# Optimization experiments

Hardware: AMD Instinct MI355X
Metric: run time of the kernel (lower is better)

Reference implementation:

```python
import jax, jax.numpy as jnp
import numpy as np

N_NODES = 50000
N_EDGES = 640000
D = 128
BN_EPS = 1e-5


def setup_inputs() -> dict:
    key = jax.random.key(0)
    k1, k2, k3 = jax.random.split(key, 3)
    x = jax.random.normal(k1, (N_NODES, D), dtype=jnp.float32)
    # Glorot-ish weight for GCNConv linear
    W = jax.random.normal(k2, (D, D), dtype=jnp.float32) * (1.0 / np.sqrt(D))
    b = jnp.zeros((D,), dtype=jnp.float32)
    gamma = jnp.ones((D,), dtype=jnp.float32)
    beta = jnp.zeros((D,), dtype=jnp.float32)
    edge_index = jax.random.randint(k3, (2, N_EDGES), 0, N_NODES, dtype=jnp.int64)
    return {"x": x, "W": W, "b": b, "gamma": gamma, "beta": beta, "edge_index": edge_index}


def reference(x, W, b, gamma, beta, edge_index):
    N = x.shape[0]
    # --- GCNConv: x' = D^{-1/2} (A + I) D^{-1/2} (x W) + b ---
    xw = x @ W  # [N, D]
    loops = jnp.arange(N, dtype=edge_index.dtype)
    src = jnp.concatenate([edge_index[0], loops])  # [E+N]
    dst = jnp.concatenate([edge_index[1], loops])
    ones = jnp.ones(src.shape[0], dtype=x.dtype)
    deg = jax.ops.segment_sum(ones, dst, num_segments=N)  # in-degree incl. self-loop
    dinv = jnp.where(deg > 0, jax.lax.rsqrt(deg), 0.0)
    norm = dinv[src] * dinv[dst]  # [E+N]
    msg = xw[src] * norm[:, None]  # [E+N, D] gathered + scaled messages
    h = jax.ops.segment_sum(msg, dst, num_segments=N) + b  # scatter-add aggregation
    # --- BatchNorm1d (training-mode batch stats over nodes, biased var) ---
    mean = jnp.mean(h, axis=0)
    var = jnp.mean(jnp.square(h - mean), axis=0)
    h = (h - mean) * jax.lax.rsqrt(var + BN_EPS) * gamma + beta
    # --- activation (relu) ---
    h = jax.nn.relu(h)
    # --- residual (in_channels == out_channels) ---
    h = x + h
    # --- dropout: identity in eval mode for deterministic reference ---
    return h
```

## Files before the change

kernel.cpp:

```cpp
#include <hip/hip_runtime.h>

#define DCH 128
#define ROWS 16
#define BN_EPS 1e-5f

typedef unsigned short u16;
typedef __attribute__((ext_vector_type(8))) short short8;
typedef __attribute__((ext_vector_type(4))) float floatx4;
typedef __attribute__((ext_vector_type(2))) unsigned uint2v;

__device__ __forceinline__ float bf2f(u16 u) {
    return __uint_as_float(((unsigned)u) << 16);
}
__device__ __forceinline__ u16 f2bf(float f) {
    unsigned u = __float_as_uint(f);
    u += 0x7FFFu + ((u >> 16) & 1u);
    return (u16)(u >> 16);
}
__device__ __forceinline__ float ldf(const void* p, int i, int isbf) {
    return isbf ? bf2f(((const u16*)p)[i]) : ((const float*)p)[i];
}

__global__ void prep_kernel(const int* ei, int ewords, const u16* xw, int* ws_i,
                            const void* W, u16* Wb, float* zbase, int zn) {
    int t = threadIdx.x;
    __shared__ int s_nz, s_hits;
    if (t == 0) { s_nz = 0; s_hits = 0; }
    __syncthreads();
    if (blockIdx.x == 0) {
        int nz = 0;
        for (int i = t; i < 1024; i += 256) {
            int w = 2 * i + 1;
            if (w < ewords) nz |= ei[w];
        }
        if (nz) atomicOr(&s_nz, 1);
    }
    unsigned m = (xw[2 * t] >> 8) & 0x7F;
    if (m >= 0x3B && m <= 0x43) atomicAdd(&s_hits, 1);
    __syncthreads();
    int isbf = (s_hits >= 128) ? 1 : 0;
    if (blockIdx.x == 0 && t == 0) {
        ws_i[0] = (s_nz == 0) ? 1 : 0;
        ws_i[1] = isbf;
        ws_i[2] = 0;
    }
    int gstride = gridDim.x * 256;
    for (int idx = blockIdx.x * 256 + t; idx < DCH * DCH; idx += gstride) {
        int j = idx & 7, lane = (idx >> 3) & 63, kk = (idx >> 9) & 3, nt = idx >> 11;
        int k = kk * 32 + (lane >> 4) * 8 + j;
        int n = nt * 16 + (lane & 15);
        Wb[idx] = f2bf(ldf(W, k * DCH + n, isbf));
    }
    for (int i = blockIdx.x * 256 + t; i < zn; i += gstride) zbase[i] = 0.f;
}

__global__ void zero_kernel(float* p, int n) {
    int stride = gridDim.x * 256;
    for (int i = blockIdx.x * 256 + threadIdx.x; i < n; i += stride) p[i] = 0.f;
}

__global__ void paint_kernel(u16* out, int n, unsigned val) {
    int stride = gridDim.x * 256;
    for (int i = blockIdx.x * 256 + threadIdx.x; i < n; i += stride) out[i] = (u16)val;
}

__global__ void detect_kernel(const int* ei, int ewords, const u16* xw, int* ws_i) {
    __shared__ int s_nz, s_hits;
    int t = threadIdx.x;
    if (t == 0) { s_nz = 0; s_hits = 0; }
    __syncthreads();
    int nz = 0;
    for (int i = t; i < 1024; i += 256) {
        int w = 2 * i + 1;
        if (w < ewords) nz |= ei[w];
    }
    if (nz) atomicOr(&s_nz, 1);
    unsigned m = (xw[2 * t] >> 8) & 0x7F;
    if (m >= 0x3B && m <= 0x43) atomicAdd(&s_hits, 1);
    __syncthreads();
    if (t == 0) {
        ws_i[0] = (s_nz == 0) ? 1 : 0;
        ws_i[1] = (s_hits >= 128) ? 1 : 0;
        ws_i[2] = 0;
    }
}

__global__ void deg_kernel(const int* ei, int E, int* ws_i, int* deg, int N) {
    int is64 = ws_i[0];
    int i = blockIdx.x * 256 + threadIdx.x;
    if (i < E) {
        int s = is64 ? ei[2 * i] : ei[i];
        int d = is64 ? ei[2 * E + 2 * i] : ei[E + i];
        if (((unsigned)s >= (unsigned)N) || ((unsigned)d >= (unsigned)N))
            atomicOr(&ws_i[2], 2);
        d = min(max(d, 0), N - 1);
        atomicAdd(&deg[d], 1);
    }
}

__global__ void dinv_kernel(const int* deg, float* dinv, int N, int* ws_i) {
    int i = blockIdx.x * 256 + threadIdx.x;
    if (i < N) {
        float v = rsqrtf((float)(deg[i] + 1));
        if (!(v > 0.f && v <= 1.001f)) atomicOr(&ws_i[2], 4);
        dinv[i] = v;
    }
}

__global__ void scanA_kernel(const int* deg, int* part, int N) {
    int base = blockIdx.x * 1024 + threadIdx.x * 4;
    int s = 0;
    #pragma unroll
    for (int j = 0; j < 4; ++j) {
        int i = base + j;
        if (i < N) s += deg[i];
    }
    #pragma unroll
    for (int o = 1; o < 64; o <<= 1) s += __shfl_xor(s, o, 64);
    __shared__ int ws4[4];
    if ((threadIdx.x & 63) == 0) ws4[threadIdx.x >> 6] = s;
    __syncthreads();
    if (threadIdx.x == 0) part[blockIdx.x] = ws4[0] + ws4[1] + ws4[2] + ws4[3];
}

__global__ void scanB_kernel(int* part, int P) {
    __shared__ int wsum[4];
    int t = threadIdx.x, lane = t & 63, w = t >> 6;
    int v = (t < P) ? part[t] : 0;
    int sc = v;
    #pragma unroll
    for (int o = 1; o < 64; o <<= 1) {
        int u = __shfl_up(sc, o, 64);
        if (lane >= o) sc += u;
    }
    if (lane == 63) wsum[w] = sc;
    __syncthreads();
    if (t < 4) {
        int s = wsum[t];
        #pragma unroll
        for (int o = 1; o < 4; o <<= 1) {
            int u = __shfl_up(s, o, 4);
            if (t >= o) s += u;
        }
        wsum[t] = s;
    }
    __syncthreads();
    int excl = sc - v + (w ? wsum[w - 1] : 0);
    if (t < P) part[t] = excl;
}

__global__ void scanC_kernel(int* deg_cursor, const int* part, int* rowptr,
                             float* dinv, int N) {
    __shared__ int wsum[4];
    int t = threadIdx.x, lane = t & 63, w = t >> 6;
    int base = blockIdx.x * 1024 + t * 4;
    int v[4], ts = 0;
    #pragma unroll
    for (int j = 0; j < 4; ++j) {
        int i = base + j;
        v[j] = (i < N) ? deg_cursor[i] : 0;
        ts += v[j];
    }
    int sc = ts;
    #pragma unroll
    for (int o = 1; o < 64; o <<= 1) {
        int u = __shfl_up(sc, o, 64);
        if (lane >= o) sc += u;
    }
    if (lane == 63) wsum[w] = sc;
    __syncthreads();
    if (t < 4) {
        int s = wsum[t];
        #pragma unroll
        for (int o = 1; o < 4; o <<= 1) {
            int u = __shfl_up(s, o, 4);
            if (t >= o) s += u;
        }
        wsum[t] = s;
    }
    __syncthreads();
    int run = sc - ts + (w ? wsum[w - 1] : 0) + part[blockIdx.x];
    #pragma unroll
    for (int j = 0; j < 4; ++j) {
        int i = base + j;
        if (i < N) {
            deg_cursor[i] = run;
            run += v[j];
            rowptr[i + 1] = run;
            dinv[i] = rsqrtf((float)(v[j] + 1));
        }
    }
    if (blockIdx.x == 0 && t == 0) rowptr[0] = 0;
}

__global__ void fillcsr_kernel(const int* ei, int E, const int* ws_i,
                               int* cursor, int* col, int N) {
    int is64 = ws_i[0];
    int i = blockIdx.x * 256 + threadIdx.x;
    if (i < E) {
        int s = is64 ? ei[2 * i] : ei[i];
        int d = is64 ? ei[2 * E + 2 * i] : ei[E + i];
        s = min(max(s, 0), N - 1);
        d = min(max(d, 0), N - 1);
        int pos = atomicAdd(&cursor[d], 1);
        col[pos] = s;
    }
}

__global__ void gemm_mfma_kernel(const void* x, const u16* Wb, const float* dinv,
                                 const int* ws_i, u16* y, int N) {
    int isbf = ws_i[1];
    int t = threadIdx.x;
    int wv = t >> 6, lane = t & 63;
    int quad = lane >> 4, l16 = lane & 15;
    int r0 = blockIdx.x * 64 + wv * 16;
    int rl = min(r0 + l16, N - 1);
    short8 a[4];
    if (isbf) {
        const u16* xp = (const u16*)x + (size_t)rl * DCH + quad * 8;
        #pragma unroll
        for (int kk = 0; kk < 4; ++kk)
            a[kk] = *(const short8*)(xp + kk * 32);
    } else {
        const float* xp = (const float*)x + (size_t)rl * DCH + quad * 8;
        #pragma unroll
        for (int kk = 0; kk < 4; ++kk) {
            float4 f0 = *(const float4*)(xp + kk * 32);
            float4 f1 = *(const float4*)(xp + kk * 32 + 4);
            short8 aa;
            aa[0] = (short)f2bf(f0.x); aa[1] = (short)f2bf(f0.y);
            aa[2] = (short)f2bf(f0.z); aa[3] = (short)f2bf(f0.w);
            aa[4] = (short)f2bf(f1.x); aa[5] = (short)f2bf(f1.y);
            aa[6] = (short)f2bf(f1.z); aa[7] = (short)f2bf(f1.w);
            a[kk] = aa;
        }
    }
    floatx4 acc[8];
    #pragma unroll
    for (int i = 0; i < 8; ++i) acc[i] = (floatx4)(0.f);
    #pragma unroll
    for (int nt = 0; nt < 8; ++nt) {
        #pragma unroll
        for (int kk = 0; kk < 4; ++kk) {
            short8 bfr = *(const short8*)&Wb[(((nt << 2) | kk) * 64 + lane) * 8];
            acc[nt] = __builtin_amdgcn_mfma_f32_16x16x32_bf16(a[kk], bfr, acc[nt], 0, 0, 0);
        }
    }
    #pragma unroll
    for (int i = 0; i < 4; ++i) {
        int row = r0 + quad * 4 + i;
        if (row < N) {
            float dv = dinv[row];
            #pragma unroll
            for (int nt = 0; nt < 8; ++nt)
                y[(size_t)row * DCH + nt * 16 + l16] = f2bf(acc[nt][i] * dv);
        }
    }
}

__global__ __launch_bounds__(256, 4)
void gather_stats_kernel(const int* rowptr, const int* col, const u16* y,
                         const float* dinv, const void* b, const int* ws_i,
                         float* h, float* sums, float* sumsq, int N) {
    int isbf = ws_i[1];
    int t = threadIdx.x;
    int hw = t >> 5;
    int l32 = t & 31;
    int c0 = l32 * 4;
    float bb[4];
    #pragma unroll
    for (int k = 0; k < 4; ++k) bb[k] = ldf(b, c0 + k, isbf);
    float ps[4] = {0.f, 0.f, 0.f, 0.f}, pq[4] = {0.f, 0.f, 0.f, 0.f};
    int stream_id = blockIdx.x * 8 + hw;
    int nstreams = gridDim.x * 8;

    int n = stream_id;
    int beg = 0, end = 0;
    uint2v qs = (uint2v)(0u);
    if (n < N) {
        beg = rowptr[n];
        end = rowptr[n + 1];
        qs = *(const uint2v*)&y[(size_t)n * DCH + c0];
    }
    while (n < N) {
        int n2 = n + nstreams;
        int begN = 0, endN = 0;
        uint2v qsN = (uint2v)(0u);
        if (n2 < N) {
            begN = rowptr[n2];
            endN = rowptr[n2 + 1];
            qsN = *(const uint2v*)&y[(size_t)n2 * DCH + c0];
        }

        float a0[4] = { bf2f((u16)(qs.x & 0xFFFF)), bf2f((u16)(qs.x >> 16)),
                        bf2f((u16)(qs.y & 0xFFFF)), bf2f((u16)(qs.y >> 16)) };
        float a1[4] = {0.f, 0.f, 0.f, 0.f};
        float a2[4] = {0.f, 0.f, 0.f, 0.f};
        float a3[4] = {0.f, 0.f, 0.f, 0.f};
        int j = beg;
        int s0 = 0, s1 = 0, s2 = 0, s3 = 0, s4 = 0, s5 = 0, s6 = 0, s7 = 0;
        bool have8 = (j + 7 < end);
        if (have8) {
            s0 = __builtin_nontemporal_load(col + j);
            s1 = __builtin_nontemporal_load(col + j + 1);
            s2 = __builtin_nontemporal_load(col + j + 2);
            s3 = __builtin_nontemporal_load(col + j + 3);
            s4 = __builtin_nontemporal_load(col + j + 4);
            s5 = __builtin_nontemporal_load(col + j + 5);
            s6 = __builtin_nontemporal_load(col + j + 6);
            s7 = __builtin_nontemporal_load(col + j + 7);
        }
        while (have8) {
            uint2v q0 = *(const uint2v*)&y[(size_t)s0 * DCH + c0];
            uint2v q1 = *(const uint2v*)&y[(size_t)s1 * DCH + c0];
            uint2v q2 = *(const uint2v*)&y[(size_t)s2 * DCH + c0];
            uint2v q3 = *(const uint2v*)&y[(size_t)s3 * DCH + c0];
            uint2v q4 = *(const uint2v*)&y[(size_t)s4 * DCH + c0];
            uint2v q5 = *(const uint2v*)&y[(size_t)s5 * DCH + c0];
            uint2v q6 = *(const uint2v*)&y[(size_t)s6 * DCH + c0];
            uint2v q7 = *(const uint2v*)&y[(size_t)s7 * DCH + c0];
            int jn = j + 8;
            bool haven = (jn + 7 < end);
            if (haven) {
                s0 = __builtin_nontemporal_load(col + jn);
                s1 = __builtin_nontemporal_load(col + jn + 1);
                s2 = __builtin_nontemporal_load(col + jn + 2);
                s3 = __builtin_nontemporal_load(col + jn + 3);
                s4 = __builtin_nontemporal_load(col + jn + 4);
                s5 = __builtin_nontemporal_load(col + jn + 5);
                s6 = __builtin_nontemporal_load(col + jn + 6);
                s7 = __builtin_nontemporal_load(col + jn + 7);
            }
            a0[0] += bf2f((u16)(q0.x & 0xFFFF)); a0[1] += bf2f((u16)(q0.x >> 16));
            a0[2] += bf2f((u16)(q0.y & 0xFFFF)); a0[3] += bf2f((u16)(q0.y >> 16));
            a1[0] += bf2f((u16)(q1.x & 0xFFFF)); a1[1] += bf2f((u16)(q1.x >> 16));
            a1[2] += bf2f((u16)(q1.y & 0xFFFF)); a1[3] += bf2f((u16)(q1.y >> 16));
            a2[0] += bf2f((u16)(q2.x & 0xFFFF)); a2[1] += bf2f((u16)(q2.x >> 16));
            a2[2] += bf2f((u16)(q2.y & 0xFFFF)); a2[3] += bf2f((u16)(q2.y >> 16));
            a3[0] += bf2f((u16)(q3.x & 0xFFFF)); a3[1] += bf2f((u16)(q3.x >> 16));
            a3[2] += bf2f((u16)(q3.y & 0xFFFF)); a3[3] += bf2f((u16)(q3.y >> 16));
            a0[0] += bf2f((u16)(q4.x & 0xFFFF)); a0[1] += bf2f((u16)(q4.x >> 16));
            a0[2] += bf2f((u16)(q4.y & 0xFFFF)); a0[3] += bf2f((u16)(q4.y >> 16));
            a1[0] += bf2f((u16)(q5.x & 0xFFFF)); a1[1] += bf2f((u16)(q5.x >> 16));
            a1[2] += bf2f((u16)(q5.y & 0xFFFF)); a1[3] += bf2f((u16)(q5.y >> 16));
            a2[0] += bf2f((u16)(q6.x & 0xFFFF)); a2[1] += bf2f((u16)(q6.x >> 16));
            a2[2] += bf2f((u16)(q6.y & 0xFFFF)); a2[3] += bf2f((u16)(q6.y >> 16));
            a3[0] += bf2f((u16)(q7.x & 0xFFFF)); a3[1] += bf2f((u16)(q7.x >> 16));
            a3[2] += bf2f((u16)(q7.y & 0xFFFF)); a3[3] += bf2f((u16)(q7.y >> 16));
            j = jn; have8 = haven;
        }
        if (j + 3 < end) {
            s0 = __builtin_nontemporal_load(col + j);
            s1 = __builtin_nontemporal_load(col + j + 1);
            s2 = __builtin_nontemporal_load(col + j + 2);
            s3 = __builtin_nontemporal_load(col + j + 3);
            uint2v q0 = *(const uint2v*)&y[(size_t)s0 * DCH + c0];
            uint2v q1 = *(const uint2v*)&y[(size_t)s1 * DCH + c0];
            uint2v q2 = *(const uint2v*)&y[(size_t)s2 * DCH + c0];
            uint2v q3 = *(const uint2v*)&y[(size_t)s3 * DCH + c0];
            a0[0] += bf2f((u16)(q0.x & 0xFFFF)); a0[1] += bf2f((u16)(q0.x >> 16));
            a0[2] += bf2f((u16)(q0.y & 0xFFFF)); a0[3] += bf2f((u16)(q0.y >> 16));
            a1[0] += bf2f((u16)(q1.x & 0xFFFF)); a1[1] += bf2f((u16)(q1.x >> 16));
            a1[2] += bf2f((u16)(q1.y & 0xFFFF)); a1[3] += bf2f((u16)(q1.y >> 16));
            a2[0] += bf2f((u16)(q2.x & 0xFFFF)); a2[1] += bf2f((u16)(q2.x >> 16));
            a2[2] += bf2f((u16)(q2.y & 0xFFFF)); a2[3] += bf2f((u16)(q2.y >> 16));
            a3[0] += bf2f((u16)(q3.x & 0xFFFF)); a3[1] += bf2f((u16)(q3.x >> 16));
            a3[2] += bf2f((u16)(q3.y & 0xFFFF)); a3[3] += bf2f((u16)(q3.y >> 16));
            j += 4;
        }
        for (; j < end; ++j) {
            uint2v q0 = *(const uint2v*)&y[(size_t)__builtin_nontemporal_load(col + j) * DCH + c0];
            a0[0] += bf2f((u16)(q0.x & 0xFFFF)); a0[1] += bf2f((u16)(q0.x >> 16));
            a0[2] += bf2f((u16)(q0.y & 0xFFFF)); a0[3] += bf2f((u16)(q0.y >> 16));
        }
        float dn = dinv[n];
        floatx4 o;
        o[0] = fmaf((a0[0] + a1[0]) + (a2[0] + a3[0]), dn, bb[0]);
        o[1] = fmaf((a0[1] + a1[1]) + (a2[1] + a3[1]), dn, bb[1]);
        o[2] = fmaf((a0[2] + a1[2]) + (a2[2] + a3[2]), dn, bb[2]);
        o[3] = fmaf((a0[3] + a1[3]) + (a2[3] + a3[3]), dn, bb[3]);
        __builtin_nontemporal_store(o, (floatx4*)&h[(size_t)n * DCH + c0]);
        ps[0] += o[0]; pq[0] += o[0] * o[0];
        ps[1] += o[1]; pq[1] += o[1] * o[1];
        ps[2] += o[2]; pq[2] += o[2] * o[2];
        ps[3] += o[3]; pq[3] += o[3] * o[3];

        n = n2; beg = begN; end = endN; qs = qsN;
    }
    __shared__ float lps[8][DCH], lpq[8][DCH];
    #pragma unroll
    for (int k = 0; k < 4; ++k) { lps[hw][c0 + k] = ps[k]; lpq[hw][c0 + k] = pq[k]; }
    __syncthreads();
    if (t < DCH) {
        int ch = (t + blockIdx.x * 16) & 127;
        float s = 0.f, q = 0.f;
        #pragma unroll
        for (int i = 0; i < 8; ++i) { s += lps[i][ch]; q += lpq[i][ch]; }
        atomicAdd(&sums[ch], s);
        atomicAdd(&sumsq[ch], q);
    }
}

__global__ void gemm_valu_kernel(const void* x, const void* W, const float* dinv,
                                 const int* ws_i, void* y, int N) {
    __shared__ float WsF[64 * DCH];
    __shared__ float xs[ROWS * DCH];
    int isbf = ws_i[1];
    int t = threadIdx.x;
    int r0 = blockIdx.x * ROWS;
    for (int i = t; i < ROWS * DCH; i += 256) {
        int r = r0 + (i >> 7);
        xs[i] = (r < N) ? ldf(x, r * DCH + (i & 127), isbf) : 0.f;
    }
    int d = t & 127, rh = t >> 7;
    float s[8];
    #pragma unroll
    for (int j = 0; j < 8; ++j) s[j] = 0.f;
    for (int half = 0; half < 2; ++half) {
        __syncthreads();
        for (int i = t; i < 64 * DCH; i += 256)
            WsF[i] = ldf(W, half * 64 * DCH + i, isbf);
        __syncthreads();
        #pragma unroll
        for (int j = 0; j < 8; ++j) {
            int rr = rh + 2 * j;
            float a = s[j];
            #pragma unroll 16
            for (int k = 0; k < 64; ++k)
                a = fmaf(xs[rr * DCH + half * 64 + k], WsF[k * DCH + d], a);
            s[j] = a;
        }
    }
    #pragma unroll
    for (int j = 0; j < 8; ++j) {
        int r = r0 + rh + 2 * j;
        if (r < N) {
            float v = s[j] * dinv[r];
            if (isbf) ((u16*)y)[r * DCH + d] = f2bf(v);
            else      ((float*)y)[r * DCH + d] = v;
        }
    }
}

__global__ void scatter_kernel(const int* ei, int E, const int* ws_i,
                               const void* y, float* acc, int N) {
    int is64 = ws_i[0], isbf = ws_i[1];
    int gid = blockIdx.x * 256 + threadIdx.x;
    int e = gid >> 5;
    if (e >= E) return;
    int c0 = (gid & 31) * 4;
    int s = is64 ? ei[2 * e] : ei[e];
    int d = is64 ? ei[2 * E + 2 * e] : ei[E + e];
    s = min(max(s, 0), N - 1);
    d = min(max(d, 0), N - 1);
    float v0, v1, v2, v3;
    if (isbf) {
        uint2 raw = *(const uint2*)&((const u16*)y)[s * DCH + c0];
        v0 = bf2f((u16)(raw.x & 0xFFFF)); v1 = bf2f((u16)(raw.x >> 16));
        v2 = bf2f((u16)(raw.y & 0xFFFF)); v3 = bf2f((u16)(raw.y >> 16));
    } else {
        float4 raw = *(const float4*)&((const float*)y)[s * DCH + c0];
        v0 = raw.x; v1 = raw.y; v2 = raw.z; v3 = raw.w;
    }
    float* a = &acc[d * DCH + c0];
    atomicAdd(a + 0, v0);
    atomicAdd(a + 1, v1);
    atomicAdd(a + 2, v2);
    atomicAdd(a + 3, v3);
}

__global__ void bnstat_kernel(const void* y, float* acc, const float* dinv,
                              const void* b, int* ws_i,
                              float* sums, float* sumsq, int total) {
    int isbf = ws_i[1];
    int t = threadIdx.x;
    int d = t & 127;
    float bb = ldf(b, d, isbf);
    float ps = 0.f, pq = 0.f;
    int stride = gridDim.x * 256;
    for (int i = blockIdx.x * 256 + t; i < total; i += stride) {
        int r = i >> 7;
        float yv = isbf ? bf2f(((const u16*)y)[i]) : ((const float*)y)[i];
        float v = (yv + acc[i]) * dinv[r] + bb;
        acc[i] = v;
        ps += v;
        pq += v * v;
    }
    __shared__ float ls[256], lq[256];
    ls[t] = ps; lq[t] = pq;
    __syncthreads();
    if (t < 128) {
        atomicAdd(&sums[d], ls[t] + ls[t + 128]);
        atomicAdd(&sumsq[d], lq[t] + lq[t + 128]);
    }
}

__global__ void out_kernel(const float* h, const void* x,
                           const void* gamma, const void* beta,
                           int* ws_i, const float* sums, const float* sumsq,
                           void* out, int total, float invN) {
    __shared__ float sc[DCH], sh[DCH];
    int isbf = ws_i[1];
    int t = threadIdx.x;
    if (t < DCH) {
        float mean = sums[t] * invN;
        float var = fmaxf(sumsq[t] * invN - mean * mean, 0.f);
        float s = ldf(gamma, t, isbf) * rsqrtf(var + BN_EPS);
        if (!(var < 1e8f && fabsf(s) < 1e6f)) atomicOr(&ws_i[2], 32);
        sc[t] = s;
        sh[t] = ldf(beta, t, isbf) - mean * s;
    }
    __syncthreads();
    int total4 = total >> 2;
    int stride = gridDim.x * 256;
    int i0 = blockIdx.x * 256 + t;
    int d0 = (i0 << 2) & 127;
    float c0 = sc[d0], c1 = sc[d0 + 1], c2 = sc[d0 + 2], c3 = sc[d0 + 3];
    float f0 = sh[d0], f1 = sh[d0 + 1], f2 = sh[d0 + 2], f3 = sh[d0 + 3];
    if (isbf) {
        for (int i = i0; i < total4; i += stride) {
            floatx4 hv = __builtin_nontemporal_load((const floatx4*)h + i);
            uint2v xv = __builtin_nontemporal_load((const uint2v*)x + i);
            float v0 = fmaxf(fmaf(hv[0], c0, f0), 0.f) + bf2f((u16)(xv.x & 0xFFFF));
            float v1 = fmaxf(fmaf(hv[1], c1, f1), 0.f) + bf2f((u16)(xv.x >> 16));
            float v2 = fmaxf(fmaf(hv[2], c2, f2), 0.f) + bf2f((u16)(xv.y & 0xFFFF));
            float v3 = fmaxf(fmaf(hv[3], c3, f3), 0.f) + bf2f((u16)(xv.y >> 16));
            uint2v o;
            o.x = (unsigned)f2bf(v0) | ((unsigned)f2bf(v1) << 16);
            o.y = (unsigned)f2bf(v2) | ((unsigned)f2bf(v3) << 16);
            __builtin_nontemporal_store(o, (uint2v*)out + i);
        }
    } else {
        for (int i = i0; i < total4; i += stride) {
            floatx4 hv = __builtin_nontemporal_load((const floatx4*)h + i);
            floatx4 xv = __builtin_nontemporal_load((const floatx4*)x + i);
            floatx4 o;
            o[0] = fmaxf(fmaf(hv[0], c0, f0), 0.f) + xv[0];
            o[1] = fmaxf(fmaf(hv[1], c1, f1), 0.f) + xv[1];
            o[2] = fmaxf(fmaf(hv[2], c2, f2), 0.f) + xv[2];
            o[3] = fmaxf(fmaf(hv[3], c3, f3), 0.f) + xv[3];
            __builtin_nontemporal_store(o, (floatx4*)out + i);
        }
    }
    for (int i = (total4 << 2) + i0; i < total; i += stride) {
        int d = i & 127;
        float v = fmaxf(fmaf(h[i], sc[d], sh[d]), 0.f);
        if (isbf) ((u16*)out)[i] = f2bf(v + bf2f(((const u16*)x)[i]));
        else      ((float*)out)[i] = v + ((const float*)x)[i];
    }
}

__global__ void diag_kernel(const int* ws_i, void* out, int n) {
    int e = ws_i[2];
    if (!e) return;
    int isbf = ws_i[1];
    float v = 4096.f + 32.f * (float)(e & 63);
    int stride = gridDim.x * 256;
    if (isbf) {
        u16 code = f2bf(v);
        for (int i = blockIdx.x * 256 + threadIdx.x; i < n; i += stride)
            ((u16*)out)[i] = code;
    } else {
        for (int i = blockIdx.x * 256 + threadIdx.x; i < n; i += stride)
            ((float*)out)[i] = v;
    }
}

extern "C" void kernel_launch(void* const* d_in, const int* in_sizes, int n_in,
                              void* d_out, int out_size, void* d_ws, size_t ws_size,
                              hipStream_t stream) {
    const void* x     = d_in[0];
    const void* W     = d_in[1];
    const void* b     = d_in[2];
    const void* gamma = d_in[3];
    const void* beta  = d_in[4];
    const int*  ei    = (const int*)d_in[5];

    const int N  = in_sizes[0] / DCH;
    const int E  = in_sizes[5] / 2;
    const int ND = N * DCH;
    const int P  = (N + 1023) / 1024;

    char* wsb = (char*)d_ws;
    int*  ws_i = (int*)wsb;

    size_t o_wb   = 64;
    size_t o_deg  = o_wb + 32768;
    size_t o_sum  = o_deg + 4 * (size_t)N;
    size_t o_sq   = o_sum + 512;
    size_t o_rp   = o_sq + 512;
    size_t o_dinv = o_rp + 4 * ((size_t)N + 1) + 4;
    size_t o_part = o_dinv + 4 * (size_t)N;
    size_t o_h    = (o_part + 1024 + 255) & ~(size_t)255;
    size_t o_col  = o_h + 4 * (size_t)ND;
    size_t need_csr = o_col + 4 * (size_t)E;

    (void)hipGetLastError();

    if (ws_size >= need_csr) {
        u16*   Wb    = (u16*)(wsb + o_wb);
        int*   deg   = (int*)(wsb + o_deg);
        float* sums  = (float*)(wsb + o_sum);
        float* sumsq = (float*)(wsb + o_sq);
        int*   rowptr= (int*)(wsb + o_rp);
        float* dinv  = (float*)(wsb + o_dinv);
        int*   part  = (int*)(wsb + o_part);
        float* h     = (float*)(wsb + o_h);
        int*   col   = (int*)(wsb + o_col);
        u16*   y     = (u16*)d_out;

        prep_kernel<<<128, 256, 0, stream>>>(ei, 2 * E, (const u16*)x, ws_i,
                                             W, Wb, (float*)(wsb + o_deg), N + 256);
        deg_kernel<<<(E + 255) / 256, 256, 0, stream>>>(ei, E, ws_i, deg, N);
        scanA_kernel<<<P, 256, 0, stream>>>(deg, part, N);
        scanB_kernel<<<1, 256, 0, stream>>>(part, P);
        scanC_kernel<<<P, 256, 0, stream>>>(deg, part, rowptr, dinv, N);
        fillcsr_kernel<<<(E + 255) / 256, 256, 0, stream>>>(ei, E, ws_i, deg, col, N);
        gemm_mfma_kernel<<<(N + 63) / 64, 256, 0, stream>>>(x, Wb, dinv, ws_i, y, N);
        gather_stats_kernel<<<1024, 256, 0, stream>>>(rowptr, col, y, dinv, b, ws_i,
                                                      h, sums, sumsq, N);
        out_kernel<<<2048, 256, 0, stream>>>(h, x, gamma, beta, ws_i, sums, sumsq,
                                             d_out, ND, 1.0f / (float)N);
        diag_kernel<<<512, 256, 0, stream>>>(ws_i, d_out, out_size);
    } else {
        int*   deg   = (int*)(wsb + 16);
        float* dinv  = (float*)(wsb + 16 + 4 * (size_t)N);
        float* sums  = (float*)(wsb + 16 + 8 * (size_t)N);
        float* sumsq = sums + DCH;
        float* acc   = sumsq + DCH;
        size_t need = 16 + 8 * (size_t)N + 1024 + 4 * (size_t)ND;
        if (ws_size < need) {
            int mb = (int)(ws_size >> 20); if (mb > 127) mb = 127;
            float v = 2048.f + 16.f * (float)mb;
            unsigned u; __builtin_memcpy(&u, &v, 4);
            paint_kernel<<<1024, 256, 0, stream>>>((u16*)d_out, out_size, u >> 16);
            return;
        }
        detect_kernel<<<1, 256, 0, stream>>>(ei, 2 * E, (const u16*)x, ws_i);
        zero_kernel<<<2048, 256, 0, stream>>>((float*)(wsb + 16), 2 * N + 256 + ND);
        deg_kernel<<<(E + 255) / 256, 256, 0, stream>>>(ei, E, ws_i, deg, N);
        dinv_kernel<<<(N + 255) / 256, 256, 0, stream>>>(deg, dinv, N, ws_i);
        gemm_valu_kernel<<<(N + ROWS - 1) / ROWS, 256, 0, stream>>>(x, W, dinv, ws_i, d_out, N);
        scatter_kernel<<<(E * 32 + 255) / 256, 256, 0, stream>>>(ei, E, ws_i, d_out, acc, N);
        bnstat_kernel<<<240, 256, 0, stream>>>(d_out, acc, dinv, b, ws_i, sums, sumsq, ND);
        out_kernel<<<256, 256, 0, stream>>>(acc, x, gamma, beta, ws_i, sums, sumsq,
                                            d_out, ND, 1.0f / (float)N);
        diag_kernel<<<512, 256, 0, stream>>>(ws_i, d_out, out_size);
    }

    if (hipGetLastError() != hipSuccess)
        hipMemsetAsync(d_out, 0x42, (size_t)out_size * 2, stream);
}
```

Baseline: 240.2 us.

## Fuse gather, BN stats and output via grid barrier; merge scan passes; vectorize edge reads

Merges the gather/stats kernel with the BatchNorm apply and output kernel, using a software grid-wide barrier. The first eight node rows per stream stay in registers, so h is only written and re-read for any leftover rows. It also folds the single-block part scan into scanC, where each block sums the preceding partials itself. deg and fillcsr now read int64 edge pairs as int4 vectors, two edges per thread. This removes two launches and most of the h round trip through memory. The risks are higher register pressure and a deadlock if all 1024 blocks cannot be co-resident for the barrier.

```diff
diff --git a/kernel.cpp b/kernel.cpp
--- a/kernel.cpp
+++ b/kernel.cpp
@@ -43,6 +43,8 @@
         ws_i[0] = (s_nz == 0) ? 1 : 0;
         ws_i[1] = isbf;
         ws_i[2] = 0;
+        ws_i[8] = 0;
+        ws_i[9] = 0;
     }
     int gstride = gridDim.x * 256;
     for (int idx = blockIdx.x * 256 + t; idx < DCH * DCH; idx += gstride) {
@@ -88,7 +90,19 @@
 __global__ void deg_kernel(const int* ei, int E, int* ws_i, int* deg, int N) {
     int is64 = ws_i[0];
     int i = blockIdx.x * 256 + threadIdx.x;
-    if (i < E) {
+    if (is64 && !(E & 1)) {
+        if (2 * i < E) {
+            int4 sp = ((const int4*)ei)[i];
+            int4 dp = ((const int4*)(ei + 2 * E))[i];
+            if (((unsigned)sp.x >= (unsigned)N) || ((unsigned)dp.x >= (unsigned)N) ||
+                ((unsigned)sp.z >= (unsigned)N) || ((unsigned)dp.z >= (unsigned)N))
+                atomicOr(&ws_i[2], 2);
+            int d0 = min(max(dp.x, 0), N - 1);
+            int d1 = min(max(dp.z, 0), N - 1);
+            atomicAdd(&deg[d0], 1);
+            atomicAdd(&deg[d1], 1);
+        }
+    } else if (i < E) {
         int s = is64 ? ei[2 * i] : ei[i];
         int d = is64 ? ei[2 * E + 2 * i] : ei[E + i];
         if (((unsigned)s >= (unsigned)N) || ((unsigned)d >= (unsigned)N))
@@ -123,11 +137,24 @@
     if (threadIdx.x == 0) part[blockIdx.x] = ws4[0] + ws4[1] + ws4[2] + ws4[3];
 }
 
-__global__ void scanB_kernel(int* part, int P) {
-    __shared__ int wsum[4];
+__global__ void scanC_kernel(int* deg_cursor, const int* part, int* rowptr,
+                             float* dinv, int N, int P) {
+    __shared__ int wsum[4], wsP[4];
     int t = threadIdx.x, lane = t & 63, w = t >> 6;
-    int v = (t < P) ? part[t] : 0;
-    int sc = v;
+    int pv = (t < P && t < (int)blockIdx.x) ? part[t] : 0;
+    #pragma unroll
+    for (int o = 1; o < 64; o <<= 1) pv += __shfl_xor(pv, o, 64);
+    if (lane == 0) wsP[w] = pv;
+
+    int base = blockIdx.x * 1024 + t * 4;
+    int v[4], ts = 0;
+    #pragma unroll
+    for (int j = 0; j < 4; ++j) {
+        int i = base + j;
+        v[j] = (i < N) ? deg_cursor[i] : 0;
+        ts += v[j];
+    }
+    int sc = ts;
     #pragma unroll
     for (int o = 1; o < 64; o <<= 1) {
         int u = __shfl_up(sc, o, 64);
@@ -145,41 +172,8 @@
         wsum[t] = s;
     }
     __syncthreads();
-    int excl = sc - v + (w ? wsum[w - 1] : 0);
-    if (t < P) part[t] = excl;
-}
-
-__global__ void scanC_kernel(int* deg_cursor, const int* part, int* rowptr,
-                             float* dinv, int N) {
-    __shared__ int wsum[4];
-    int t = threadIdx.x, lane = t & 63, w = t >> 6;
-    int base = blockIdx.x * 1024 + t * 4;
-    int v[4], ts = 0;
-    #pragma unroll
-    for (int j = 0; j < 4; ++j) {
-        int i = base + j;
-        v[j] = (i < N) ? deg_cursor[i] : 0;
-        ts += v[j];
-    }
-    int sc = ts;
-    #pragma unroll
-    for (int o = 1; o < 64; o <<= 1) {
-        int u = __shfl_up(sc, o, 64);
-        if (lane >= o) sc += u;
-    }
-    if (lane == 63) wsum[w] = sc;
-    __syncthreads();
-    if (t < 4) {
-        int s = wsum[t];
-        #pragma unroll
-        for (int o = 1; o < 4; o <<= 1) {
-            int u = __shfl_up(s, o, 4);
-            if (t >= o) s += u;
-        }
-        wsum[t] = s;
-    }
-    __syncthreads();
-    int run = sc - ts + (w ? wsum[w - 1] : 0) + part[blockIdx.x];
+    int blockbase = wsP[0] + wsP[1] + wsP[2] + wsP[3];
+    int run = sc - ts + (w ? wsum[w - 1] : 0) + blockbase;
     #pragma unroll
     for (int j = 0; j < 4; ++j) {
         int i = base + j;
@@ -197,7 +191,18 @@
                                int* cursor, int* col, int N) {
     int is64 = ws_i[0];
     int i = blockIdx.x * 256 + threadIdx.x;
-    if (i < E) {
+    if (is64 && !(E & 1)) {
+        if (2 * i < E) {
+            int4 sp = ((const int4*)ei)[i];
+            int4 dp = ((const int4*)(ei + 2 * E))[i];
+            int s0 = min(max(sp.x, 0), N - 1), d0 = min(max(dp.x, 0), N - 1);
+            int s1 = min(max(sp.z, 0), N - 1), d1 = min(max(dp.z, 0), N - 1);
+            int p0 = atomicAdd(&cursor[d0], 1);
+            col[p0] = s0;
+            int p1 = atomicAdd(&cursor[d1], 1);
+            col[p1] = s1;
+        }
+    } else if (i < E) {
         int s = is64 ? ei[2 * i] : ei[i];
         int d = is64 ? ei[2 * E + 2 * i] : ei[E + i];
         s = min(max(s, 0), N - 1);
@@ -258,10 +263,37 @@
     }
 }
 
+__device__ __forceinline__ void bn_apply_store(int nn, floatx4 hv, floatx4 scl,
+                                               floatx4 shf, int isbf, const void* x,
+                                               void* out, int c0, int N) {
+    if (nn >= N) return;
+    if (isbf) {
+        uint2v xv = *(const uint2v*)((const u16*)x + (size_t)nn * DCH + c0);
+        float v0 = fmaxf(fmaf(hv[0], scl[0], shf[0]), 0.f) + bf2f((u16)(xv.x & 0xFFFF));
+        float v1 = fmaxf(fmaf(hv[1], scl[1], shf[1]), 0.f) + bf2f((u16)(xv.x >> 16));
+        float v2 = fmaxf(fmaf(hv[2], scl[2], shf[2]), 0.f) + bf2f((u16)(xv.y & 0xFFFF));
+        float v3 = fmaxf(fmaf(hv[3], scl[3], shf[3]), 0.f) + bf2f((u16)(xv.y >> 16));
+        uint2v ov;
+        ov.x = (unsigned)f2bf(v0) | ((unsigned)f2bf(v1) << 16);
+        ov.y = (unsigned)f2bf(v2) | ((unsigned)f2bf(v3) << 16);
+        __builtin_nontemporal_store(ov, (uint2v*)((u16*)out + (size_t)nn * DCH + c0));
+    } else {
+        floatx4 xv = *(const floatx4*)((const float*)x + (size_t)nn * DCH + c0);
+        floatx4 ov;
+        ov[0] = fmaxf(fmaf(hv[0], scl[0], shf[0]), 0.f) + xv[0];
+        ov[1] = fmaxf(fmaf(hv[1], scl[1], shf[1]), 0.f) + xv[1];
+        ov[2] = fmaxf(fmaf(hv[2], scl[2], shf[2]), 0.f) + xv[2];
+        ov[3] = fmaxf(fmaf(hv[3], scl[3], shf[3]), 0.f) + xv[3];
+        __builtin_nontemporal_store(ov, (floatx4*)((float*)out + (size_t)nn * DCH + c0));
+    }
+}
+
 __global__ __launch_bounds__(256, 4)
-void gather_stats_kernel(const int* rowptr, const int* col, const u16* y,
-                         const float* dinv, const void* b, const int* ws_i,
-                         float* h, float* sums, float* sumsq, int N) {
+void gather_bn_out_kernel(const int* rowptr, const int* col, const u16* y,
+                          const float* dinv, const void* b, const void* x,
+                          const void* gamma, const void* beta, int* ws_i,
+                          float* h, float* sums, float* sumsq, unsigned* bar,
+                          void* out, int N, float invN) {
     int isbf = ws_i[1];
     int t = threadIdx.x;
     int hw = t >> 5;
@@ -274,6 +306,10 @@
     int stream_id = blockIdx.x * 8 + hw;
     int nstreams = gridDim.x * 8;
 
+    floatx4 hr0 = (floatx4)(0.f), hr1 = (floatx4)(0.f), hr2 = (floatx4)(0.f),
+            hr3 = (floatx4)(0.f), hr4 = (floatx4)(0.f), hr5 = (floatx4)(0.f),
+            hr6 = (floatx4)(0.f), hr7 = (floatx4)(0.f);
+    int it = 0;
     int n = stream_id;
     int beg = 0, end = 0;
     uint2v qs = (uint2v)(0u);
@@ -379,7 +415,18 @@
         o[1] = fmaf((a0[1] + a1[1]) + (a2[1] + a3[1]), dn, bb[1]);
         o[2] = fmaf((a0[2] + a1[2]) + (a2[2] + a3[2]), dn, bb[2]);
         o[3] = fmaf((a0[3] + a1[3]) + (a2[3] + a3[3]), dn, bb[3]);
-        __builtin_nontemporal_store(o, (floatx4*)&h[(size_t)n * DCH + c0]);
+        switch (it) {
+            case 0: hr0 = o; break;
+            case 1: hr1 = o; break;
+            case 2: hr2 = o; break;
+            case 3: hr3 = o; break;
+            case 4: hr4 = o; break;
+            case 5: hr5 = o; break;
+            case 6: hr6 = o; break;
+            case 7: hr7 = o; break;
+            default: __builtin_nontemporal_store(o, (floatx4*)&h[(size_t)n * DCH + c0]); break;
+        }
+        ++it;
         ps[0] += o[0]; pq[0] += o[0] * o[0];
         ps[1] += o[1]; pq[1] += o[1] * o[1];
         ps[2] += o[2]; pq[2] += o[2] * o[2];
@@ -398,6 +445,43 @@
         for (int i = 0; i < 8; ++i) { s += lps[i][ch]; q += lpq[i][ch]; }
         atomicAdd(&sums[ch], s);
         atomicAdd(&sumsq[ch], q);
+    }
+    __syncthreads();
+    if (t == 0) {
+        __threadfence();
+        unsigned a = __hip_atomic_fetch_add(bar, 1u, __ATOMIC_ACQ_REL, __HIP_MEMORY_SCOPE_AGENT);
+        if (a == gridDim.x - 1)
+            __hip_atomic_store(bar + 1, 1u, __ATOMIC_RELEASE, __HIP_MEMORY_SCOPE_AGENT);
+        else
+            while (!__hip_atomic_load(bar + 1, __ATOMIC_ACQUIRE, __HIP_MEMORY_SCOPE_AGENT))
+                __builtin_amdgcn_s_sleep(16);
+    }
+    __syncthreads();
+    floatx4 scl, shf;
+    bool bad = false;
+    #pragma unroll
+    for (int k = 0; k < 4; ++k) {
+        float s = __hip_atomic_load(&sums[c0 + k], __ATOMIC_RELAXED, __HIP_MEMORY_SCOPE_AGENT);
+        float q = __hip_atomic_load(&sumsq[c0 + k], __ATOMIC_RELAXED, __HIP_MEMORY_SCOPE_AGENT);
+        float mean = s * invN;
+        float var = fmaxf(q * invN - mean * mean, 0.f);
+        float sc = ldf(gamma, c0 + k, isbf) * rsqrtf(var + BN_EPS);
+        if (!(var < 1e8f && fabsf(sc) < 1e6f)) bad = true;
+        scl[k] = sc;
+        shf[k] = ldf(beta, c0 + k, isbf) - mean * sc;
+    }
+    if (bad) atomicOr(&ws_i[2], 32);
+    bn_apply_store(stream_id + 0 * nstreams, hr0, scl, shf, isbf, x, out, c0, N);
+    bn_apply_store(stream_id + 1 * nstreams, hr1, scl, shf, isbf, x, out, c0, N);
+    bn_apply_store(stream_id + 2 * nstreams, hr2, scl, shf, isbf, x, out, c0, N);
+    bn_apply_store(stream_id + 3 * nstreams, hr3, scl, shf, isbf, x, out, c0, N);
+    bn_apply_store(stream_id + 4 * nstreams, hr4, scl, shf, isbf, x, out, c0, N);
+    bn_apply_store(stream_id + 5 * nstreams, hr5, scl, shf, isbf, x, out, c0, N);
+    bn_apply_store(stream_id + 6 * nstreams, hr6, scl, shf, isbf, x, out, c0, N);
+    bn_apply_store(stream_id + 7 * nstreams, hr7, scl, shf, isbf, x, out, c0, N);
+    for (int nn = stream_id + 8 * nstreams; nn < N; nn += nstreams) {
+        floatx4 hv = *(const floatx4*)&h[(size_t)nn * DCH + c0];
+        bn_apply_store(nn, hv, scl, shf, isbf, x, out, c0, N);
     }
 }
 
@@ -597,7 +681,7 @@
 
     (void)hipGetLastError();
 
-    if (ws_size >= need_csr) {
+    if (ws_size >= need_csr && P <= 256) {
         u16*   Wb    = (u16*)(wsb + o_wb);
         int*   deg   = (int*)(wsb + o_deg);
         float* sums  = (float*)(wsb + o_sum);
@@ -613,14 +697,13 @@
                                              W, Wb, (float*)(wsb + o_deg), N + 256);
         deg_kernel<<<(E + 255) / 256, 256, 0, stream>>>(ei, E, ws_i, deg, N);
         scanA_kernel<<<P, 256, 0, stream>>>(deg, part, N);
-        scanB_kernel<<<1, 256, 0, stream>>>(part, P);
-        scanC_kernel<<<P, 256, 0, stream>>>(deg, part, rowptr, dinv, N);
+        scanC_kernel<<<P, 256, 0, stream>>>(deg, part, rowptr, dinv, N, P);
         fillcsr_kernel<<<(E + 255) / 256, 256, 0, stream>>>(ei, E, ws_i, deg, col, N);
         gemm_mfma_kernel<<<(N + 63) / 64, 256, 0, stream>>>(x, Wb, dinv, ws_i, y, N);
-        gather_stats_kernel<<<1024, 256, 0, stream>>>(rowptr, col, y, dinv, b, ws_i,
-                                                      h, sums, sumsq, N);
-        out_kernel<<<2048, 256, 0, stream>>>(h, x, gamma, beta, ws_i, sums, sumsq,
-                                             d_out, ND, 1.0f / (float)N);
+        gather_bn_out_kernel<<<1024, 256, 0, stream>>>(rowptr, col, y, dinv, b, x,
+                                                       gamma, beta, ws_i, h, sums, sumsq,
+                                                       (unsigned*)wsb + 8, d_out, N,
+                                                       1.0f / (float)N);
         diag_kernel<<<512, 256, 0, stream>>>(ws_i, d_out, out_size);
     } else {
         int*   deg   = (int*)(wsb + 16);
```

Result: slower. 393.6 us (+63.9%).

## Fuse degree count into prep kernel, fold scanB into scanC, vectorize edge loads

Applied to the files above, without the earlier changes.

Merges the format detection, weight repacking and degree histogram into one kernel, and replaces the separate zeroing inside prep with a small zero kernel. Removes the single-block scanB launch by having each scanC block sum the preceding partials itself. Reads int64 edge pairs as int4 vectors in the degree and CSR fill passes and adds bounds guards. The aim is fewer launches and fewer serialized small kernels. The cost is that every prep block now repeats the detection reads, and each scanC block re-reduces up to 256 partials.

```diff
diff --git a/kernel.cpp b/kernel.cpp
--- a/kernel.cpp
+++ b/kernel.cpp
@@ -21,47 +21,66 @@
     return isbf ? bf2f(((const u16*)p)[i]) : ((const float*)p)[i];
 }
 
-__global__ void prep_kernel(const int* ei, int ewords, const u16* xw, int* ws_i,
-                            const void* W, u16* Wb, float* zbase, int zn) {
+__global__ void zero_kernel(float* p, int n) {
+    int stride = gridDim.x * 256;
+    for (int i = blockIdx.x * 256 + threadIdx.x; i < n; i += stride) p[i] = 0.f;
+}
+
+__global__ void paint_kernel(u16* out, int n, unsigned val) {
+    int stride = gridDim.x * 256;
+    for (int i = blockIdx.x * 256 + threadIdx.x; i < n; i += stride) out[i] = (u16)val;
+}
+
+__global__ void prep_deg_kernel(const int* ei, int E, const u16* xw, int* ws_i,
+                                const void* W, u16* Wb, int* deg, int N) {
     int t = threadIdx.x;
     __shared__ int s_nz, s_hits;
     if (t == 0) { s_nz = 0; s_hits = 0; }
     __syncthreads();
-    if (blockIdx.x == 0) {
-        int nz = 0;
-        for (int i = t; i < 1024; i += 256) {
-            int w = 2 * i + 1;
-            if (w < ewords) nz |= ei[w];
-        }
-        if (nz) atomicOr(&s_nz, 1);
-    }
+    int ewords = 2 * E;
+    int nz = 0;
+    for (int i = t; i < 1024; i += 256) {
+        int w = 2 * i + 1;
+        if (w < ewords) nz |= ei[w];
+    }
+    if (nz) atomicOr(&s_nz, 1);
     unsigned m = (xw[2 * t] >> 8) & 0x7F;
     if (m >= 0x3B && m <= 0x43) atomicAdd(&s_hits, 1);
     __syncthreads();
+    int is64 = (s_nz == 0) ? 1 : 0;
     int isbf = (s_hits >= 128) ? 1 : 0;
     if (blockIdx.x == 0 && t == 0) {
-        ws_i[0] = (s_nz == 0) ? 1 : 0;
+        ws_i[0] = is64;
         ws_i[1] = isbf;
-        ws_i[2] = 0;
-    }
-    int gstride = gridDim.x * 256;
-    for (int idx = blockIdx.x * 256 + t; idx < DCH * DCH; idx += gstride) {
+    }
+    int gid = blockIdx.x * 256 + t;
+    int gthreads = gridDim.x * 256;
+    for (int idx = gid; idx < DCH * DCH; idx += gthreads) {
         int j = idx & 7, lane = (idx >> 3) & 63, kk = (idx >> 9) & 3, nt = idx >> 11;
         int k = kk * 32 + (lane >> 4) * 8 + j;
         int n = nt * 16 + (lane & 15);
         Wb[idx] = f2bf(ldf(W, k * DCH + n, isbf));
     }
-    for (int i = blockIdx.x * 256 + t; i < zn; i += gstride) zbase[i] = 0.f;
-}
-
-__global__ void zero_kernel(float* p, int n) {
-    int stride = gridDim.x * 256;
-    for (int i = blockIdx.x * 256 + threadIdx.x; i < n; i += stride) p[i] = 0.f;
-}
-
-__global__ void paint_kernel(u16* out, int n, unsigned val) {
-    int stride = gridDim.x * 256;
-    for (int i = blockIdx.x * 256 + threadIdx.x; i < n; i += stride) out[i] = (u16)val;
+    if (is64 && !(E & 1)) {
+        int P2 = E >> 1;
+        for (int p = gid; p < P2; p += gthreads) {
+            int4 sp = ((const int4*)ei)[p];
+            int4 dp = ((const int4*)(ei + 2 * E))[p];
+            if (((unsigned)sp.x >= (unsigned)N) || ((unsigned)dp.x >= (unsigned)N) ||
+                ((unsigned)sp.z >= (unsigned)N) || ((unsigned)dp.z >= (unsigned)N))
+                atomicOr(&ws_i[2], 2);
+            atomicAdd(&deg[min(max(dp.x, 0), N - 1)], 1);
+            atomicAdd(&deg[min(max(dp.z, 0), N - 1)], 1);
+        }
+    } else {
+        for (int e = gid; e < E; e += gthreads) {
+            int s = is64 ? ei[2 * e] : ei[e];
+            int d = is64 ? ei[2 * E + 2 * e] : ei[E + e];
+            if (((unsigned)s >= (unsigned)N) || ((unsigned)d >= (unsigned)N))
+                atomicOr(&ws_i[2], 2);
+            atomicAdd(&deg[min(max(d, 0), N - 1)], 1);
+        }
+    }
 }
 
 __global__ void detect_kernel(const int* ei, int ewords, const u16* xw, int* ws_i) {
@@ -123,11 +142,24 @@
     if (threadIdx.x == 0) part[blockIdx.x] = ws4[0] + ws4[1] + ws4[2] + ws4[3];
 }
 
-__global__ void scanB_kernel(int* part, int P) {
-    __shared__ int wsum[4];
+__global__ void scanC_kernel(int* deg_cursor, const int* part, int* rowptr,
+                             float* dinv, int N, int P) {
+    __shared__ int wsum[4], wsP[4];
     int t = threadIdx.x, lane = t & 63, w = t >> 6;
-    int v = (t < P) ? part[t] : 0;
-    int sc = v;
+    int pv = (t < P && t < (int)blockIdx.x) ? part[t] : 0;
+    #pragma unroll
+    for (int o = 1; o < 64; o <<= 1) pv += __shfl_xor(pv, o, 64);
+    if (lane == 0) wsP[w] = pv;
+
+    int base = blockIdx.x * 1024 + t * 4;
+    int v[4], ts = 0;
+    #pragma unroll
+    for (int j = 0; j < 4; ++j) {
+        int i = base + j;
+        v[j] = (i < N) ? deg_cursor[i] : 0;
+        ts += v[j];
+    }
+    int sc = ts;
     #pragma unroll
     for (int o = 1; o < 64; o <<= 1) {
         int u = __shfl_up(sc, o, 64);
@@ -145,41 +177,8 @@
         wsum[t] = s;
     }
     __syncthreads();
-    int excl = sc - v + (w ? wsum[w - 1] : 0);
-    if (t < P) part[t] = excl;
-}
-
-__global__ void scanC_kernel(int* deg_cursor, const int* part, int* rowptr,
-                             float* dinv, int N) {
-    __shared__ int wsum[4];
-    int t = threadIdx.x, lane = t & 63, w = t >> 6;
-    int base = blockIdx.x * 1024 + t * 4;
-    int v[4], ts = 0;
-    #pragma unroll
-    for (int j = 0; j < 4; ++j) {
-        int i = base + j;
-        v[j] = (i < N) ? deg_cursor[i] : 0;
-        ts += v[j];
-    }
-    int sc = ts;
-    #pragma unroll
-    for (int o = 1; o < 64; o <<= 1) {
-        int u = __shfl_up(sc, o, 64);
-        if (lane >= o) sc += u;
-    }
-    if (lane == 63) wsum[w] = sc;
-    __syncthreads();
-    if (t < 4) {
-        int s = wsum[t];
-        #pragma unroll
-        for (int o = 1; o < 4; o <<= 1) {
-            int u = __shfl_up(s, o, 4);
-            if (t >= o) s += u;
-        }
-        wsum[t] = s;
-    }
-    __syncthreads();
-    int run = sc - ts + (w ? wsum[w - 1] : 0) + part[blockIdx.x];
+    int blockbase = wsP[0] + wsP[1] + wsP[2] + wsP[3];
+    int run = sc - ts + (w ? wsum[w - 1] : 0) + blockbase;
     #pragma unroll
     for (int j = 0; j < 4; ++j) {
         int i = base + j;
@@ -197,13 +196,24 @@
                                int* cursor, int* col, int N) {
     int is64 = ws_i[0];
     int i = blockIdx.x * 256 + threadIdx.x;
-    if (i < E) {
+    if (is64 && !(E & 1)) {
+        if (2 * i < E) {
+            int4 sp = ((const int4*)ei)[i];
+            int4 dp = ((const int4*)(ei + 2 * E))[i];
+            int s0 = min(max(sp.x, 0), N - 1), d0 = min(max(dp.x, 0), N - 1);
+            int s1 = min(max(sp.z, 0), N - 1), d1 = min(max(dp.z, 0), N - 1);
+            int p0 = atomicAdd(&cursor[d0], 1);
+            if ((unsigned)p0 < (unsigned)E) col[p0] = s0;
+            int p1 = atomicAdd(&cursor[d1], 1);
+            if ((unsigned)p1 < (unsigned)E) col[p1] = s1;
+        }
+    } else if (i < E) {
         int s = is64 ? ei[2 * i] : ei[i];
         int d = is64 ? ei[2 * E + 2 * i] : ei[E + i];
         s = min(max(s, 0), N - 1);
         d = min(max(d, 0), N - 1);
         int pos = atomicAdd(&cursor[d], 1);
-        col[pos] = s;
+        if ((unsigned)pos < (unsigned)E) col[pos] = s;
     }
 }
 
@@ -597,7 +607,7 @@
 
     (void)hipGetLastError();
 
-    if (ws_size >= need_csr) {
+    if (ws_size >= need_csr && P <= 256) {
         u16*   Wb    = (u16*)(wsb + o_wb);
         int*   deg   = (int*)(wsb + o_deg);
         float* sums  = (float*)(wsb + o_sum);
@@ -609,12 +619,11 @@
         int*   col   = (int*)(wsb + o_col);
         u16*   y     = (u16*)d_out;
 
-        prep_kernel<<<128, 256, 0, stream>>>(ei, 2 * E, (const u16*)x, ws_i,
-                                             W, Wb, (float*)(wsb + o_deg), N + 256);
-        deg_kernel<<<(E + 255) / 256, 256, 0, stream>>>(ei, E, ws_i, deg, N);
+        zero_kernel<<<128, 256, 0, stream>>>((float*)wsb, (int)((o_sq + 512) / 4));
+        prep_deg_kernel<<<1250, 256, 0, stream>>>(ei, E, (const u16*)x, ws_i,
+                                                  W, Wb, deg, N);
         scanA_kernel<<<P, 256, 0, stream>>>(deg, part, N);
-        scanB_kernel<<<1, 256, 0, stream>>>(part, P);
-        scanC_kernel<<<P, 256, 0, stream>>>(deg, part, rowptr, dinv, N);
+        scanC_kernel<<<P, 256, 0, stream>>>(deg, part, rowptr, dinv, N, P);
         fillcsr_kernel<<<(E + 255) / 256, 256, 0, stream>>>(ei, E, ws_i, deg, col, N);
         gemm_mfma_kernel<<<(N + 63) / 64, 256, 0, stream>>>(x, Wb, dinv, ws_i, y, N);
         gather_stats_kernel<<<1024, 256, 0, stream>>>(rowptr, col, y, dinv, b, ws_i,
```

Measured after the change: 237.5 us. About the same (-1.1%).
